# Kernel optimization log

Measured on AMD Instinct MI355X. Metric: run time of the kernel, lower is better.

Reference implementation:

```python
import jax, jax.numpy as jnp
import numpy as np

N_NODES = 100000
N_EDGES = 3200000
N_ELEMS = 10


def setup_inputs() -> dict:
    key = jax.random.key(0)
    k1, k2, k3, k4, k5 = jax.random.split(key, 5)
    # edge distances in (0.1, 5.1) Angstrom, shape [E, 1]
    x = jax.random.uniform(k1, (N_EDGES, 1), dtype=jnp.float32) * 5.0 + 0.1
    # one-hot-ish node element encoding; only argmax matters
    node_attrs = jax.random.normal(k2, (N_NODES, N_ELEMS), dtype=jnp.float32)
    edge_index = jax.random.randint(k3, (2, N_EDGES), 0, N_NODES)
    # atomic numbers of the chemical species present (1..89)
    atomic_numbers = jax.random.randint(k4, (N_ELEMS,), 1, 90)
    # stand-in for ase.data.covalent_radii (119 entries, ~0.3..2.3 A)
    covalent_radii = jax.random.uniform(k5, (119,), dtype=jnp.float32) * 2.0 + 0.3
    return {
        "x": x,
        "node_attrs": node_attrs,
        "edge_index": edge_index,
        "atomic_numbers": atomic_numbers,
        "covalent_radii": covalent_radii,
    }


def _polynomial_envelope(x, r_max, p):
    # PolynomialCutoff.calculate_envelope, p = 6
    r = x / r_max
    env = (1.0
           - (p + 1.0) * (p + 2.0) / 2.0 * jnp.power(r, p)
           + p * (p + 2.0) * jnp.power(r, p + 1)
           - p * (p + 1.0) / 2.0 * jnp.power(r, p + 2))
    return env * (x < r_max)


def reference(x, node_attrs, edge_index, atomic_numbers, covalent_radii):
    c = jnp.array([0.1818, 0.5099, 0.2802, 0.02817], dtype=jnp.float32)
    p = 6.0
    a_exp = jnp.float32(0.3)
    a_prefactor = jnp.float32(0.4543)

    sender, receiver = edge_index[0], edge_index[1]
    # per-node atomic number from one-hot attrs, [N, 1]
    node_Z = atomic_numbers[jnp.argmax(node_attrs, axis=1)][..., None]
    Z_u = node_Z[sender].astype(jnp.int32)  # [E, 1]
    Z_v = node_Z[receiver].astype(jnp.int32)  # [E, 1]
    Zu_f = Z_u.astype(jnp.float32)
    Zv_f = Z_v.astype(jnp.float32)

    a = a_prefactor * 0.529 / (jnp.power(Zu_f, a_exp) + jnp.power(Zv_f, a_exp))
    r_over_a = x / a  # [E, 1]
    phi = (c[0] * jnp.exp(-3.2 * r_over_a)
           + c[1] * jnp.exp(-0.9423 * r_over_a)
           + c[2] * jnp.exp(-0.4028 * r_over_a)
           + c[3] * jnp.exp(-0.2016 * r_over_a))
    v_edges = 14.3996 * Zu_f * Zv_f / x * phi  # [E, 1]

    r_max = covalent_radii[Z_u] + covalent_radii[Z_v]  # [E, 1]
    envelope = _polynomial_envelope(x, r_max, p)
    v_edges = 0.5 * v_edges * envelope  # [E, 1]

    # scatter-sum edge energies into receiver nodes -> [N]
    V_ZBL = jax.ops.segment_sum(v_edges[:, 0], receiver,
                                num_segments=node_attrs.shape[0])
    return V_ZBL
```

## Files before the change

### kernel.cpp

```cpp
#include <hip/hip_runtime.h>
#include <stdint.h>

#define N_NODES 100000
#define N_ELEM4 50000
#define N_EDGES 3200000
#define N_ELEMS 10
#define N_PAIRS (N_ELEMS * N_ELEMS)

#define NB 256
#define NPB 391
#define SCAT_THREADS 1024
#define NBLK 512
#define EPB 6256
#define NGROUPS (EPB / 4)
#define NG4 (N_EDGES / 4)
#define PREP_BLOCKS 196

#define L_REC   0
#define L_ELEM  25024
#define L_TAB   (25024 + 50000)
#define L_CNT   (L_TAB + 1600)
#define L_OFF   (L_CNT + 1024)
#define LDS_BYTES (L_OFF + 1024)

__global__ __launch_bounds__(256) void prep_kernel(
    const float* __restrict__ node_attrs,
    const int* __restrict__ atomic_numbers,
    const float* __restrict__ covalent_radii,
    uint8_t* __restrict__ node_elem4,
    float4* __restrict__ pair_tab) {
  int i = blockIdx.x * 256 + threadIdx.x;

  if (blockIdx.x == 0 && threadIdx.x < N_PAIRS) {
    int t = threadIdx.x;
    int eu = t / N_ELEMS, ev = t % N_ELEMS;
    float Zuf = (float)atomic_numbers[eu];
    float Zvf = (float)atomic_numbers[ev];
    float a = 0.4543f * 0.529f / (powf(Zuf, 0.3f) + powf(Zvf, 0.3f));
    float rmax = covalent_radii[(int)Zuf] + covalent_radii[(int)Zvf];
    pair_tab[t] = make_float4(1.0f / a, 0.5f * 14.3996f * Zuf * Zvf,
                              rmax, 1.0f / rmax);
  }

  if (i < N_ELEM4) {
    unsigned int packed = 0;
#pragma unroll
    for (int h = 0; h < 2; ++h) {
      int node = 2 * i + h;
      const float2* row = (const float2*)(node_attrs + (size_t)node * N_ELEMS);
      float best = -INFINITY;
      int bj = 0;
#pragma unroll
      for (int k = 0; k < 5; ++k) {
        float2 v = row[k];
        if (v.x > best) { best = v.x; bj = 2 * k; }
        if (v.y > best) { best = v.y; bj = 2 * k + 1; }
      }
      packed |= (unsigned int)bj << (h * 4);
    }
    node_elem4[i] = (uint8_t)packed;
  }
}

__device__ __forceinline__ int elem_of(const uint8_t* s_elem4, int n) {
  return (s_elem4[n >> 1] >> ((n & 1) * 4)) & 0xF;
}

__device__ __forceinline__ float edge_val(float xi, int u, int v,
                                          const uint8_t* s_elem4,
                                          const float4* s_tab) {
  int eu = elem_of(s_elem4, u);
  int ev = elem_of(s_elem4, v);
  float4 tb = s_tab[eu * N_ELEMS + ev];
  float roa = xi * tb.x;
  float phi = 0.1818f  * __expf(-3.2f    * roa)
            + 0.5099f  * __expf(-0.9423f * roa)
            + 0.2802f  * __expf(-0.4028f * roa)
            + 0.02817f * __expf(-0.2016f * roa);
  float val = tb.y * phi / xi;
  float r  = xi * tb.w;
  float r2 = r * r;
  float r6 = r2 * r2 * r2;
  float env = 1.0f - 28.0f * r6 + 48.0f * r6 * r - 21.0f * r6 * r2;
  return (xi < tb.z) ? val * env : 0.0f;
}

__global__ __launch_bounds__(SCAT_THREADS) void scatter_kernel(
    const float* __restrict__ x,
    const int* __restrict__ edge_index,
    const uint8_t* __restrict__ node_elem4,
    const float4* __restrict__ pair_tab,
    unsigned int* __restrict__ dir,
    unsigned int* __restrict__ records) {
  extern __shared__ char smem[];
  unsigned int* s_rec   = (unsigned int*)(smem + L_REC);
  uint8_t*      s_elem4 = (uint8_t*)(smem + L_ELEM);
  float4*       s_tab   = (float4*)(smem + L_TAB);
  unsigned int* s_cnt   = (unsigned int*)(smem + L_CNT);
  unsigned int* s_off   = (unsigned int*)(smem + L_OFF);

  int tid = threadIdx.x;

  {
    const uint4* src = (const uint4*)node_elem4;
    uint4* dst = (uint4*)s_elem4;
    for (int j = tid; j < N_ELEM4 / 16; j += SCAT_THREADS) dst[j] = src[j];
  }
  if (tid < N_PAIRS) s_tab[tid] = pair_tab[tid];
  if (tid < NB) s_cnt[tid] = 0u;
  __syncthreads();

  float val[8];
  unsigned int pk[8];

#pragma unroll
  for (int k = 0; k < 2; ++k) {
    int gl = k * SCAT_THREADS + tid;
    int g  = blockIdx.x * NGROUPS + gl;
    bool ok = (gl < NGROUPS) && (g < NG4);
    int e = g * 4;
    float4 xv = make_float4(1, 1, 1, 1);
    int4 uu = make_int4(0, 0, 0, 0), vv = make_int4(0, 0, 0, 0);
    if (ok) {
      xv = *(const float4*)(x + e);
      uu = *(const int4*)(edge_index + e);
      vv = *(const int4*)(edge_index + N_EDGES + e);
    }
    int rv[4] = {vv.x, vv.y, vv.z, vv.w};
    int ru[4] = {uu.x, uu.y, uu.z, uu.w};
    float xs[4] = {xv.x, xv.y, xv.z, xv.w};
#pragma unroll
    for (int c = 0; c < 4; ++c) {
      int j = k * 4 + c;
      if (ok) {
        val[j] = edge_val(xs[c], ru[c], rv[c], s_elem4, s_tab);
        unsigned int b = (unsigned int)rv[c] / NPB;
        unsigned int lid = (unsigned int)rv[c] - b * NPB;
        unsigned int r = atomicAdd(&s_cnt[b], 1u);
        pk[j] = (b << 22) | (r << 9) | lid;
      } else {
        pk[j] = 0xFFFFFFFFu;
      }
    }
  }
  __syncthreads();

  if (tid < 64) {
    unsigned int c0 = s_cnt[tid * 4 + 0];
    unsigned int c1 = s_cnt[tid * 4 + 1];
    unsigned int c2 = s_cnt[tid * 4 + 2];
    unsigned int c3 = s_cnt[tid * 4 + 3];
    unsigned int local = c0 + c1 + c2 + c3;
    unsigned int inc = local;
#pragma unroll
    for (int d = 1; d < 64; d <<= 1) {
      unsigned int t = __shfl_up((int)inc, d, 64);
      if (tid >= d) inc += t;
    }
    unsigned int excl = inc - local;
    s_off[tid * 4 + 0] = excl;
    s_off[tid * 4 + 1] = excl + c0;
    s_off[tid * 4 + 2] = excl + c0 + c1;
    s_off[tid * 4 + 3] = excl + c0 + c1 + c2;
  }
  __syncthreads();

  if (tid < NB)
    dir[(size_t)blockIdx.x * NB + tid] = (s_off[tid] << 13) | s_cnt[tid];

#pragma unroll
  for (int j = 0; j < 8; ++j) {
    if (pk[j] != 0xFFFFFFFFu) {
      unsigned int b = pk[j] >> 22;
      unsigned int r = (pk[j] >> 9) & 0x1FFFu;
      unsigned int lid = pk[j] & 0x1FFu;
      s_rec[s_off[b] + r] = (__float_as_uint(val[j]) & ~0x1FFu) | lid;
    }
  }
  __syncthreads();

  {
    uint4* dst = (uint4*)(records + (size_t)blockIdx.x * EPB);
    const uint4* src = (const uint4*)s_rec;
    for (int j = tid; j < EPB / 4; j += SCAT_THREADS) dst[j] = src[j];
  }
}

__global__ __launch_bounds__(1024) void reduce_kernel(
    const unsigned int* __restrict__ dir,
    const unsigned int* __restrict__ records,
    float* __restrict__ out) {
  __shared__ float bins[NPB];
  int b = blockIdx.x, tid = threadIdx.x;

  if (tid < NPB) bins[tid] = 0.0f;
  __syncthreads();

  int seg = tid >> 1;
  int sub = tid & 1;
  unsigned int d = dir[(size_t)seg * NB + b];
  unsigned int c = d & 0x1FFFu;
  unsigned int o = d >> 13;
  const unsigned int* sp = records + (size_t)seg * EPB + o;
  for (unsigned int i = sub; i < c; i += 2) {
    unsigned int rec = sp[i];
    atomicAdd(&bins[rec & 0x1FFu], __uint_as_float(rec & ~0x1FFu));
  }
  __syncthreads();

  int nb0 = b * NPB;
  if (tid < NPB && nb0 + tid < N_NODES) out[nb0 + tid] = bins[tid];
}

extern "C" void kernel_launch(void* const* d_in, const int* in_sizes, int n_in,
                              void* d_out, int out_size, void* d_ws, size_t ws_size,
                              hipStream_t stream) {
  const float* x              = (const float*)d_in[0];
  const float* node_attrs     = (const float*)d_in[1];
  const int*   edge_index     = (const int*)d_in[2];
  const int*   atomic_numbers = (const int*)d_in[3];
  const float* covalent_radii = (const float*)d_in[4];
  float* out = (float*)d_out;

  char* wsp = (char*)d_ws;
  unsigned int* records    = (unsigned int*)wsp;
  unsigned int* dir        = (unsigned int*)(wsp + 12812288);
  float4*       pair_tab   = (float4*)(wsp + 13336576);
  uint8_t*      node_elem4 = (uint8_t*)(wsp + 13338176);

  prep_kernel<<<PREP_BLOCKS, 256, 0, stream>>>(
      node_attrs, atomic_numbers, covalent_radii, node_elem4, pair_tab);

  scatter_kernel<<<NBLK, SCAT_THREADS, LDS_BYTES, stream>>>(
      x, edge_index, node_elem4, pair_tab, dir, records);

  reduce_kernel<<<NB, 1024, 0, stream>>>(dir, records, out);
}
```

Measured before the change: 116.4 us.

## Scatter records into global per-bucket regions via atomic offsets, skipping zero edges

Replaces the per-block LDS staging of records and the per-block directory with a global per-bucket counter. Each block reserves space in fixed 16K-record bucket regions with one atomicAdd per bucket and writes records straight to global memory. Edges whose value is zero (beyond the cutoff) are dropped, so the reduce kernel reads only contiguous live records per bucket. This removes the LDS scan, the staging copy and the strided per-segment reads, at the cost of scattered global writes and a fixed capacity that could overflow if a bucket exceeds CAP. It also uses a hardware reciprocal instead of a divide.

```diff
diff --git a/kernel.cpp b/kernel.cpp
--- a/kernel.cpp
+++ b/kernel.cpp
@@ -15,31 +15,29 @@
 #define NGROUPS (EPB / 4)
 #define NG4 (N_EDGES / 4)
 #define PREP_BLOCKS 196
-
-#define L_REC   0
-#define L_ELEM  25024
-#define L_TAB   (25024 + 50000)
-#define L_CNT   (L_TAB + 1600)
-#define L_OFF   (L_CNT + 1024)
-#define LDS_BYTES (L_OFF + 1024)
+#define CAP 16384
 
 __global__ __launch_bounds__(256) void prep_kernel(
     const float* __restrict__ node_attrs,
     const int* __restrict__ atomic_numbers,
     const float* __restrict__ covalent_radii,
     uint8_t* __restrict__ node_elem4,
-    float4* __restrict__ pair_tab) {
+    float4* __restrict__ pair_tab,
+    unsigned int* __restrict__ g_cnt) {
   int i = blockIdx.x * 256 + threadIdx.x;
 
-  if (blockIdx.x == 0 && threadIdx.x < N_PAIRS) {
-    int t = threadIdx.x;
-    int eu = t / N_ELEMS, ev = t % N_ELEMS;
-    float Zuf = (float)atomic_numbers[eu];
-    float Zvf = (float)atomic_numbers[ev];
-    float a = 0.4543f * 0.529f / (powf(Zuf, 0.3f) + powf(Zvf, 0.3f));
-    float rmax = covalent_radii[(int)Zuf] + covalent_radii[(int)Zvf];
-    pair_tab[t] = make_float4(1.0f / a, 0.5f * 14.3996f * Zuf * Zvf,
-                              rmax, 1.0f / rmax);
+  if (blockIdx.x == 0) {
+    if (threadIdx.x < N_PAIRS) {
+      int t = threadIdx.x;
+      int eu = t / N_ELEMS, ev = t % N_ELEMS;
+      float Zuf = (float)atomic_numbers[eu];
+      float Zvf = (float)atomic_numbers[ev];
+      float a = 0.4543f * 0.529f / (powf(Zuf, 0.3f) + powf(Zvf, 0.3f));
+      float rmax = covalent_radii[(int)Zuf] + covalent_radii[(int)Zvf];
+      pair_tab[t] = make_float4(1.0f / a, 0.5f * 14.3996f * Zuf * Zvf,
+                                rmax, 1.0f / rmax);
+    }
+    if (threadIdx.x < NB) g_cnt[threadIdx.x] = 0u;
   }
 
   if (i < N_ELEM4) {
@@ -62,22 +60,18 @@
   }
 }
 
-__device__ __forceinline__ int elem_of(const uint8_t* s_elem4, int n) {
-  return (s_elem4[n >> 1] >> ((n & 1) * 4)) & 0xF;
-}
-
 __device__ __forceinline__ float edge_val(float xi, int u, int v,
                                           const uint8_t* s_elem4,
                                           const float4* s_tab) {
-  int eu = elem_of(s_elem4, u);
-  int ev = elem_of(s_elem4, v);
+  int eu = (s_elem4[u >> 1] >> ((u & 1) * 4)) & 0xF;
+  int ev = (s_elem4[v >> 1] >> ((v & 1) * 4)) & 0xF;
   float4 tb = s_tab[eu * N_ELEMS + ev];
   float roa = xi * tb.x;
   float phi = 0.1818f  * __expf(-3.2f    * roa)
             + 0.5099f  * __expf(-0.9423f * roa)
             + 0.2802f  * __expf(-0.4028f * roa)
             + 0.02817f * __expf(-0.2016f * roa);
-  float val = tb.y * phi / xi;
+  float val = tb.y * phi * __builtin_amdgcn_rcpf(xi);
   float r  = xi * tb.w;
   float r2 = r * r;
   float r6 = r2 * r2 * r2;
@@ -85,26 +79,24 @@
   return (xi < tb.z) ? val * env : 0.0f;
 }
 
-__global__ __launch_bounds__(SCAT_THREADS) void scatter_kernel(
+__global__ __launch_bounds__(SCAT_THREADS, 8) void scatter_kernel(
     const float* __restrict__ x,
     const int* __restrict__ edge_index,
     const uint8_t* __restrict__ node_elem4,
     const float4* __restrict__ pair_tab,
-    unsigned int* __restrict__ dir,
+    unsigned int* __restrict__ g_cnt,
     unsigned int* __restrict__ records) {
-  extern __shared__ char smem[];
-  unsigned int* s_rec   = (unsigned int*)(smem + L_REC);
-  uint8_t*      s_elem4 = (uint8_t*)(smem + L_ELEM);
-  float4*       s_tab   = (float4*)(smem + L_TAB);
-  unsigned int* s_cnt   = (unsigned int*)(smem + L_CNT);
-  unsigned int* s_off   = (unsigned int*)(smem + L_OFF);
+  __shared__ uint4        s_elem4_v[N_ELEM4 / 16];
+  __shared__ float4       s_tab[N_PAIRS];
+  __shared__ unsigned int s_cnt[NB];
+  __shared__ unsigned int s_goff[NB];
+  const uint8_t* s_elem4 = (const uint8_t*)s_elem4_v;
 
   int tid = threadIdx.x;
 
   {
     const uint4* src = (const uint4*)node_elem4;
-    uint4* dst = (uint4*)s_elem4;
-    for (int j = tid; j < N_ELEM4 / 16; j += SCAT_THREADS) dst[j] = src[j];
+    for (int j = tid; j < N_ELEM4 / 16; j += SCAT_THREADS) s_elem4_v[j] = src[j];
   }
   if (tid < N_PAIRS) s_tab[tid] = pair_tab[tid];
   if (tid < NB) s_cnt[tid] = 0u;
@@ -132,62 +124,37 @@
 #pragma unroll
     for (int c = 0; c < 4; ++c) {
       int j = k * 4 + c;
+      pk[j] = 0xFFFFFFFFu;
       if (ok) {
-        val[j] = edge_val(xs[c], ru[c], rv[c], s_elem4, s_tab);
-        unsigned int b = (unsigned int)rv[c] / NPB;
-        unsigned int lid = (unsigned int)rv[c] - b * NPB;
-        unsigned int r = atomicAdd(&s_cnt[b], 1u);
-        pk[j] = (b << 22) | (r << 9) | lid;
-      } else {
-        pk[j] = 0xFFFFFFFFu;
+        float v = edge_val(xs[c], ru[c], rv[c], s_elem4, s_tab);
+        if (v != 0.0f) {
+          unsigned int b = (unsigned int)rv[c] / NPB;
+          unsigned int lid = (unsigned int)rv[c] - b * NPB;
+          unsigned int r = atomicAdd(&s_cnt[b], 1u);
+          pk[j] = (b << 22) | (r << 9) | lid;
+          val[j] = v;
+        }
       }
     }
   }
   __syncthreads();
 
-  if (tid < 64) {
-    unsigned int c0 = s_cnt[tid * 4 + 0];
-    unsigned int c1 = s_cnt[tid * 4 + 1];
-    unsigned int c2 = s_cnt[tid * 4 + 2];
-    unsigned int c3 = s_cnt[tid * 4 + 3];
-    unsigned int local = c0 + c1 + c2 + c3;
-    unsigned int inc = local;
-#pragma unroll
-    for (int d = 1; d < 64; d <<= 1) {
-      unsigned int t = __shfl_up((int)inc, d, 64);
-      if (tid >= d) inc += t;
-    }
-    unsigned int excl = inc - local;
-    s_off[tid * 4 + 0] = excl;
-    s_off[tid * 4 + 1] = excl + c0;
-    s_off[tid * 4 + 2] = excl + c0 + c1;
-    s_off[tid * 4 + 3] = excl + c0 + c1 + c2;
-  }
-  __syncthreads();
-
-  if (tid < NB)
-    dir[(size_t)blockIdx.x * NB + tid] = (s_off[tid] << 13) | s_cnt[tid];
+  if (tid < NB) s_goff[tid] = atomicAdd(&g_cnt[tid], s_cnt[tid]);
+  __syncthreads();
 
 #pragma unroll
   for (int j = 0; j < 8; ++j) {
     if (pk[j] != 0xFFFFFFFFu) {
       unsigned int b = pk[j] >> 22;
       unsigned int r = (pk[j] >> 9) & 0x1FFFu;
-      unsigned int lid = pk[j] & 0x1FFu;
-      s_rec[s_off[b] + r] = (__float_as_uint(val[j]) & ~0x1FFu) | lid;
-    }
-  }
-  __syncthreads();
-
-  {
-    uint4* dst = (uint4*)(records + (size_t)blockIdx.x * EPB);
-    const uint4* src = (const uint4*)s_rec;
-    for (int j = tid; j < EPB / 4; j += SCAT_THREADS) dst[j] = src[j];
+      records[((size_t)b << 14) + s_goff[b] + r] =
+          (__float_as_uint(val[j]) & ~0x1FFu) | (pk[j] & 0x1FFu);
+    }
   }
 }
 
 __global__ __launch_bounds__(1024) void reduce_kernel(
-    const unsigned int* __restrict__ dir,
+    const unsigned int* __restrict__ g_cnt,
     const unsigned int* __restrict__ records,
     float* __restrict__ out) {
   __shared__ float bins[NPB];
@@ -196,14 +163,10 @@
   if (tid < NPB) bins[tid] = 0.0f;
   __syncthreads();
 
-  int seg = tid >> 1;
-  int sub = tid & 1;
-  unsigned int d = dir[(size_t)seg * NB + b];
-  unsigned int c = d & 0x1FFFu;
-  unsigned int o = d >> 13;
-  const unsigned int* sp = records + (size_t)seg * EPB + o;
-  for (unsigned int i = sub; i < c; i += 2) {
-    unsigned int rec = sp[i];
+  unsigned int cnt = g_cnt[b];
+  const unsigned int* rp = records + ((size_t)b << 14);
+  for (unsigned int i = tid; i < cnt; i += 1024) {
+    unsigned int rec = rp[i];
     atomicAdd(&bins[rec & 0x1FFu], __uint_as_float(rec & ~0x1FFu));
   }
   __syncthreads();
@@ -224,15 +187,15 @@
 
   char* wsp = (char*)d_ws;
   unsigned int* records    = (unsigned int*)wsp;
-  unsigned int* dir        = (unsigned int*)(wsp + 12812288);
-  float4*       pair_tab   = (float4*)(wsp + 13336576);
-  uint8_t*      node_elem4 = (uint8_t*)(wsp + 13338176);
+  unsigned int* g_cnt      = (unsigned int*)(wsp + 16777216);
+  float4*       pair_tab   = (float4*)(wsp + 16778240);
+  uint8_t*      node_elem4 = (uint8_t*)(wsp + 16779840);
 
   prep_kernel<<<PREP_BLOCKS, 256, 0, stream>>>(
-      node_attrs, atomic_numbers, covalent_radii, node_elem4, pair_tab);
-
-  scatter_kernel<<<NBLK, SCAT_THREADS, LDS_BYTES, stream>>>(
-      x, edge_index, node_elem4, pair_tab, dir, records);
-
-  reduce_kernel<<<NB, 1024, 0, stream>>>(dir, records, out);
-}
+      node_attrs, atomic_numbers, covalent_radii, node_elem4, pair_tab, g_cnt);
+
+  scatter_kernel<<<NBLK, SCAT_THREADS, 0, stream>>>(
+      x, edge_index, node_elem4, pair_tab, g_cnt, records);
+
+  reduce_kernel<<<NB, 1024, 0, stream>>>(g_cnt, records, out);
+}
```

Result: faster. 111.6 us (-4.2%).
